# Kernel optimization log

Measured on AMD Instinct MI355X. Metric: run time of the kernel, lower is better.

Reference implementation:

```python
import jax, jax.numpy as jnp
import numpy as np

N_NODES = 100000


def _spmm(rows, cols, vals, x):
    # out[i] = sum over edges e with rows[e]==i of vals[e] * x[cols[e]]
    gathered = x[cols] * vals[:, None]          # [E, F]
    return jax.ops.segment_sum(gathered, rows, num_segments=N_NODES)


def setup_inputs() -> dict:
    key = jax.random.key(0)
    ks = jax.random.split(key, 8)
    E = 3200000
    features = jax.random.normal(ks[0], (N_NODES, 128), dtype=jnp.float32)
    adj_rows = jnp.sort(jax.random.randint(ks[1], (E,), 0, N_NODES))
    adj_cols = jax.random.randint(ks[2], (E,), 0, N_NODES)
    adj_vals = jax.random.uniform(ks[3], (E,), dtype=jnp.float32)
    W1 = jax.random.normal(ks[4], (128, 128), dtype=jnp.float32) * 0.05
    b1 = jnp.zeros((128,), dtype=jnp.float32)
    W2 = jax.random.normal(ks[5], (128, 128), dtype=jnp.float32) * 0.05
    b2 = jnp.zeros((128,), dtype=jnp.float32)
    return {"features": features, "adj_rows": adj_rows, "adj_cols": adj_cols,
            "adj_vals": adj_vals, "W1": W1, "b1": b1, "W2": W2, "b2": b2}


def reference(features, adj_rows, adj_cols, adj_vals, W1, b1, W2, b2):
    # GC layer 1: adj @ (x @ W1) + b1
    h = _spmm(adj_rows, adj_cols, adj_vals, features @ W1) + b1
    h = jax.nn.relu(h)
    # GC layer 2: adj @ (h @ W2) + b2
    out = _spmm(adj_rows, adj_cols, adj_vals, h @ W2) + b2
    return out
```

## Files before the change

kernel.cpp:

```cpp
#include <hip/hip_runtime.h>
#include <type_traits>

#define FDIM 128

__device__ __forceinline__ uint16_t f2bf(float f) {
    uint32_t u = __float_as_uint(f);
    uint32_t r = (u + 0x7fffu + ((u >> 16) & 1u)) >> 16;
    return (uint16_t)r;
}
__device__ __forceinline__ uint32_t pack_bf16(float a, float b) {
    return (uint32_t)f2bf(a) | ((uint32_t)f2bf(b) << 16);
}
__device__ __forceinline__ float bflo(uint32_t u) { return __uint_as_float(u << 16); }
__device__ __forceinline__ float bfhi(uint32_t u) { return __uint_as_float(u & 0xffff0000u); }
__device__ __forceinline__ float bf2f(uint16_t h) { return __uint_as_float((uint32_t)h << 16); }

__global__ __launch_bounds__(256) void build_row_ptr_k(const int* __restrict__ rows,
                                                       int E, int N,
                                                       int* __restrict__ rp) {
    int i = blockIdx.x * 256 + threadIdx.x;
    if (i > N) return;
    int lo = 0, hi = E;
    while (lo < hi) {
        int mid = (lo + hi) >> 1;
        if (rows[mid] < i) lo = mid + 1; else hi = mid;
    }
    rp[i] = lo;
}

template <int ABF>
__global__ __launch_bounds__(256) void gemm_k(const void* __restrict__ A_,
                                              const float* __restrict__ W,
                                              uint16_t* __restrict__ C, int M) {
    using AT = typename std::conditional<ABF, uint16_t, float>::type;
    const AT* A = (const AT*)A_;

    __shared__ float Ws[128][128];
    const int t = threadIdx.x;
    const int row0 = blockIdx.x * 128;

#pragma unroll
    for (int i = 0; i < 16; ++i) {
        int f = t + i * 256;
        int k = f >> 5;
        int c = (f & 31) << 2;
        *(float4*)&Ws[k][c] = *(const float4*)&W[(k << 7) + c];
    }
    __syncthreads();

    const int ty = t >> 4;
    const int tx = t & 15;

    const AT* aptr[8];
    int grow[8];
#pragma unroll
    for (int i = 0; i < 8; ++i) {
        int gr = row0 + ty * 8 + i;
        grow[i] = gr;
        if (gr >= M) gr = M - 1;
        aptr[i] = A + (size_t)gr * FDIM;
    }

    float acc[8][8];
#pragma unroll
    for (int i = 0; i < 8; ++i)
#pragma unroll
        for (int j = 0; j < 8; ++j) acc[i][j] = 0.f;

#pragma unroll 4
    for (int k = 0; k < 128; ++k) {
        float a[8], b[8];
#pragma unroll
        for (int i = 0; i < 8; ++i) {
            if constexpr (ABF) a[i] = bf2f(aptr[i][k]);
            else               a[i] = aptr[i][k];
        }
        *(float4*)&b[0] = *(const float4*)&Ws[k][tx * 8];
        *(float4*)&b[4] = *(const float4*)&Ws[k][tx * 8 + 4];
#pragma unroll
        for (int i = 0; i < 8; ++i)
#pragma unroll
            for (int j = 0; j < 8; ++j) acc[i][j] = fmaf(a[i], b[j], acc[i][j]);
    }

#pragma unroll
    for (int i = 0; i < 8; ++i) {
        if (grow[i] < M) {
            uint32_t p[4];
#pragma unroll
            for (int j = 0; j < 4; ++j)
                p[j] = pack_bf16(acc[i][2 * j], acc[i][2 * j + 1]);
            *(uint4*)&C[(size_t)grow[i] * FDIM + tx * 8] =
                make_uint4(p[0], p[1], p[2], p[3]);
        }
    }
}

template <int RELU, int OBF>
__global__ __launch_bounds__(256) void spmm_k(const int* __restrict__ rp,
                                              const int* __restrict__ cols,
                                              const float* __restrict__ vals,
                                              const uint32_t* __restrict__ X,
                                              const float* __restrict__ bias,
                                              void* __restrict__ out, int N) {
    int wid  = (blockIdx.x * 256 + threadIdx.x) >> 6;
    int lane = threadIdx.x & 63;
    if (wid >= N) return;
    int s = __builtin_amdgcn_readfirstlane(rp[wid]);
    int e = __builtin_amdgcn_readfirstlane(rp[wid + 1]);

    float ax0 = 0.f, ay0 = 0.f, ax1 = 0.f, ay1 = 0.f;
    float ax2 = 0.f, ay2 = 0.f, ax3 = 0.f, ay3 = 0.f;
    int i = s;
    for (; i + 4 <= e; i += 4) {
        int c0 = __builtin_amdgcn_readfirstlane(cols[i]);
        int c1 = __builtin_amdgcn_readfirstlane(cols[i + 1]);
        int c2 = __builtin_amdgcn_readfirstlane(cols[i + 2]);
        int c3 = __builtin_amdgcn_readfirstlane(cols[i + 3]);
        float v0 = vals[i], v1 = vals[i + 1], v2 = vals[i + 2], v3 = vals[i + 3];
        uint32_t u0 = X[(size_t)c0 * 64 + lane];
        uint32_t u1 = X[(size_t)c1 * 64 + lane];
        uint32_t u2 = X[(size_t)c2 * 64 + lane];
        uint32_t u3 = X[(size_t)c3 * 64 + lane];
        ax0 = fmaf(v0, bflo(u0), ax0); ay0 = fmaf(v0, bfhi(u0), ay0);
        ax1 = fmaf(v1, bflo(u1), ax1); ay1 = fmaf(v1, bfhi(u1), ay1);
        ax2 = fmaf(v2, bflo(u2), ax2); ay2 = fmaf(v2, bfhi(u2), ay2);
        ax3 = fmaf(v3, bflo(u3), ax3); ay3 = fmaf(v3, bfhi(u3), ay3);
    }
    for (; i < e; ++i) {
        int c0 = __builtin_amdgcn_readfirstlane(cols[i]);
        float v0 = vals[i];
        uint32_t u0 = X[(size_t)c0 * 64 + lane];
        ax0 = fmaf(v0, bflo(u0), ax0); ay0 = fmaf(v0, bfhi(u0), ay0);
    }

    float ox = (ax0 + ax1) + (ax2 + ax3) + bias[lane * 2];
    float oy = (ay0 + ay1) + (ay2 + ay3) + bias[lane * 2 + 1];
    if (RELU) { ox = fmaxf(ox, 0.f); oy = fmaxf(oy, 0.f); }

    if constexpr (OBF) {
        ((uint32_t*)out)[(size_t)wid * 64 + lane] = pack_bf16(ox, oy);
    } else {
        *(float2*)((float*)out + (size_t)wid * FDIM + lane * 2) = make_float2(ox, oy);
    }
}

extern "C" void kernel_launch(void* const* d_in, const int* in_sizes, int n_in,
                              void* d_out, int out_size, void* d_ws, size_t ws_size,
                              hipStream_t stream) {
    const float* features = (const float*)d_in[0];
    const int*   adj_cols = (const int*)d_in[2];
    const float* adj_vals = (const float*)d_in[3];
    const float* W1       = (const float*)d_in[4];
    const float* b1       = (const float*)d_in[5];
    const float* W2       = (const float*)d_in[6];
    const float* b2       = (const float*)d_in[7];
    const int*   adj_rows = (const int*)d_in[1];

    const int N = in_sizes[0] / FDIM;
    const int E = in_sizes[1];
    float* out = (float*)d_out;

    char* ws = (char*)d_ws;
    int* rp = (int*)ws;
    size_t rp_bytes = (((size_t)(N + 1) * sizeof(int)) + 255) & ~(size_t)255;
    uint16_t* XWb = (uint16_t*)(ws + rp_bytes);
    uint16_t* Hb  = XWb + (size_t)N * FDIM;

    build_row_ptr_k<<<(N + 256) / 256, 256, 0, stream>>>(adj_rows, E, N, rp);
    gemm_k<0><<<(N + 127) / 128, 256, 0, stream>>>((const void*)features, W1, XWb, N);
    spmm_k<1, 1><<<((size_t)N * 64 + 255) / 256, 256, 0, stream>>>(
        rp, adj_cols, adj_vals, (const uint32_t*)XWb, b1, (void*)Hb, N);
    gemm_k<1><<<(N + 127) / 128, 256, 0, stream>>>((const void*)Hb, W2, XWb, N);
    spmm_k<0, 0><<<((size_t)N * 64 + 255) / 256, 256, 0, stream>>>(
        rp, adj_cols, adj_vals, (const uint32_t*)XWb, b2, (void*)out, N);
}
```

Before: 343.6 us.

## Use bf16 MFMA for dense GEMMs and software-pipeline SpMM gathers by 8

Replaces the scalar-FMA shared-memory GEMM with a bf16 MFMA (16x16x32) kernel that reads a pre-transposed bf16 copy of each weight matrix. Two small transpose kernels produce those copies. The SpMM kernel now unrolls edges by 8 and prefetches the next group's column indices so more gathers are in flight. This adds rounding of the weights and fp32 features to bf16, and the SpMM change raises register pressure.

```diff
diff --git a/kernel.cpp b/kernel.cpp
--- a/kernel.cpp
+++ b/kernel.cpp
@@ -2,6 +2,9 @@
 #include <type_traits>
 
 #define FDIM 128
+
+typedef __attribute__((ext_vector_type(8))) short short8v;
+typedef __attribute__((ext_vector_type(4))) float f32x4;
 
 __device__ __forceinline__ uint16_t f2bf(float f) {
     uint32_t u = __float_as_uint(f);
@@ -13,7 +16,6 @@
 }
 __device__ __forceinline__ float bflo(uint32_t u) { return __uint_as_float(u << 16); }
 __device__ __forceinline__ float bfhi(uint32_t u) { return __uint_as_float(u & 0xffff0000u); }
-__device__ __forceinline__ float bf2f(uint16_t h) { return __uint_as_float((uint32_t)h << 16); }
 
 __global__ __launch_bounds__(256) void build_row_ptr_k(const int* __restrict__ rows,
                                                        int E, int N,
@@ -28,70 +30,74 @@
     rp[i] = lo;
 }
 
+__global__ __launch_bounds__(256) void transpose_w_k(const float* __restrict__ W,
+                                                     uint16_t* __restrict__ Wt) {
+    int idx = blockIdx.x * 256 + threadIdx.x;
+    int k = idx >> 7, n = idx & 127;
+    Wt[n * FDIM + k] = f2bf(W[k * FDIM + n]);
+}
+
 template <int ABF>
-__global__ __launch_bounds__(256) void gemm_k(const void* __restrict__ A_,
-                                              const float* __restrict__ W,
-                                              uint16_t* __restrict__ C, int M) {
-    using AT = typename std::conditional<ABF, uint16_t, float>::type;
-    const AT* A = (const AT*)A_;
-
-    __shared__ float Ws[128][128];
+__global__ __launch_bounds__(256) void gemm_mfma_k(const void* __restrict__ A_,
+                                                   const uint16_t* __restrict__ Wt,
+                                                   uint16_t* __restrict__ C, int M) {
     const int t = threadIdx.x;
-    const int row0 = blockIdx.x * 128;
-
-#pragma unroll
-    for (int i = 0; i < 16; ++i) {
-        int f = t + i * 256;
-        int k = f >> 5;
-        int c = (f & 31) << 2;
-        *(float4*)&Ws[k][c] = *(const float4*)&W[(k << 7) + c];
-    }
-    __syncthreads();
-
-    const int ty = t >> 4;
-    const int tx = t & 15;
-
-    const AT* aptr[8];
-    int grow[8];
-#pragma unroll
-    for (int i = 0; i < 8; ++i) {
-        int gr = row0 + ty * 8 + i;
-        grow[i] = gr;
-        if (gr >= M) gr = M - 1;
-        aptr[i] = A + (size_t)gr * FDIM;
-    }
-
-    float acc[8][8];
-#pragma unroll
-    for (int i = 0; i < 8; ++i)
-#pragma unroll
-        for (int j = 0; j < 8; ++j) acc[i][j] = 0.f;
-
-#pragma unroll 4
-    for (int k = 0; k < 128; ++k) {
-        float a[8], b[8];
-#pragma unroll
-        for (int i = 0; i < 8; ++i) {
-            if constexpr (ABF) a[i] = bf2f(aptr[i][k]);
-            else               a[i] = aptr[i][k];
-        }
-        *(float4*)&b[0] = *(const float4*)&Ws[k][tx * 8];
-        *(float4*)&b[4] = *(const float4*)&Ws[k][tx * 8 + 4];
-#pragma unroll
-        for (int i = 0; i < 8; ++i)
-#pragma unroll
-            for (int j = 0; j < 8; ++j) acc[i][j] = fmaf(a[i], b[j], acc[i][j]);
-    }
-
-#pragma unroll
-    for (int i = 0; i < 8; ++i) {
-        if (grow[i] < M) {
-            uint32_t p[4];
-#pragma unroll
-            for (int j = 0; j < 4; ++j)
-                p[j] = pack_bf16(acc[i][2 * j], acc[i][2 * j + 1]);
-            *(uint4*)&C[(size_t)grow[i] * FDIM + tx * 8] =
-                make_uint4(p[0], p[1], p[2], p[3]);
+    const int w = t >> 6;
+    const int l = t & 63;
+    const int row0 = blockIdx.x * 128 + w * 32;
+
+    f32x4 acc[2][8];
+#pragma unroll
+    for (int mf = 0; mf < 2; ++mf)
+#pragma unroll
+        for (int nf = 0; nf < 8; ++nf) acc[mf][nf] = (f32x4)0.f;
+
+    const int lr = l & 15;
+    const int kg = l >> 4;
+
+#pragma unroll
+    for (int ks = 0; ks < 4; ++ks) {
+        const int k0 = ks * 32 + kg * 8;
+        short8v a[2];
+#pragma unroll
+        for (int mf = 0; mf < 2; ++mf) {
+            int r = row0 + mf * 16 + lr;
+            if (r >= M) r = M - 1;
+            if constexpr (ABF) {
+                a[mf] = *(const short8v*)((const uint16_t*)A_ + (size_t)r * FDIM + k0);
+            } else {
+                const float* ap = (const float*)A_ + (size_t)r * FDIM + k0;
+                float4 f0 = *(const float4*)(ap);
+                float4 f1 = *(const float4*)(ap + 4);
+                uint32_t p0 = pack_bf16(f0.x, f0.y), p1 = pack_bf16(f0.z, f0.w);
+                uint32_t p2 = pack_bf16(f1.x, f1.y), p3 = pack_bf16(f1.z, f1.w);
+                uint4 u = make_uint4(p0, p1, p2, p3);
+                a[mf] = *(short8v*)&u;
+            }
+        }
+#pragma unroll
+        for (int nf = 0; nf < 8; ++nf) {
+            short8v b = *(const short8v*)(Wt + (size_t)(nf * 16 + lr) * FDIM + k0);
+            acc[0][nf] = __builtin_amdgcn_mfma_f32_16x16x32_bf16(a[0], b, acc[0][nf], 0, 0, 0);
+            acc[1][nf] = __builtin_amdgcn_mfma_f32_16x16x32_bf16(a[1], b, acc[1][nf], 0, 0, 0);
+        }
+    }
+
+    const int colpar = l & 1;
+#pragma unroll
+    for (int mf = 0; mf < 2; ++mf) {
+#pragma unroll
+        for (int nf = 0; nf < 8; ++nf) {
+            int col = nf * 16 + lr;
+#pragma unroll
+            for (int j = 0; j < 4; ++j) {
+                float v = acc[mf][nf][j];
+                float pv = __shfl_xor(v, 1);
+                int row = row0 + mf * 16 + kg * 4 + j;
+                if (!colpar && row < M) {
+                    *(uint32_t*)(C + (size_t)row * FDIM + col) = pack_bf16(v, pv);
+                }
+            }
         }
     }
 }
@@ -109,33 +115,59 @@
     int s = __builtin_amdgcn_readfirstlane(rp[wid]);
     int e = __builtin_amdgcn_readfirstlane(rp[wid + 1]);
 
-    float ax0 = 0.f, ay0 = 0.f, ax1 = 0.f, ay1 = 0.f;
-    float ax2 = 0.f, ay2 = 0.f, ax3 = 0.f, ay3 = 0.f;
+    float ax[8], ay[8];
+#pragma unroll
+    for (int j = 0; j < 8; ++j) { ax[j] = 0.f; ay[j] = 0.f; }
+
+    const int nfull = (e - s) >> 3;
     int i = s;
-    for (; i + 4 <= e; i += 4) {
-        int c0 = __builtin_amdgcn_readfirstlane(cols[i]);
-        int c1 = __builtin_amdgcn_readfirstlane(cols[i + 1]);
-        int c2 = __builtin_amdgcn_readfirstlane(cols[i + 2]);
-        int c3 = __builtin_amdgcn_readfirstlane(cols[i + 3]);
-        float v0 = vals[i], v1 = vals[i + 1], v2 = vals[i + 2], v3 = vals[i + 3];
-        uint32_t u0 = X[(size_t)c0 * 64 + lane];
-        uint32_t u1 = X[(size_t)c1 * 64 + lane];
-        uint32_t u2 = X[(size_t)c2 * 64 + lane];
-        uint32_t u3 = X[(size_t)c3 * 64 + lane];
-        ax0 = fmaf(v0, bflo(u0), ax0); ay0 = fmaf(v0, bfhi(u0), ay0);
-        ax1 = fmaf(v1, bflo(u1), ax1); ay1 = fmaf(v1, bfhi(u1), ay1);
-        ax2 = fmaf(v2, bflo(u2), ax2); ay2 = fmaf(v2, bfhi(u2), ay2);
-        ax3 = fmaf(v3, bflo(u3), ax3); ay3 = fmaf(v3, bfhi(u3), ay3);
+    int cc[8];
+
+    if (nfull > 0) {
+#pragma unroll
+        for (int j = 0; j < 8; ++j) cc[j] = __builtin_amdgcn_readfirstlane(cols[i + j]);
+        for (int g = 1; g < nfull; ++g) {
+            int cn[8];
+#pragma unroll
+            for (int j = 0; j < 8; ++j) cn[j] = __builtin_amdgcn_readfirstlane(cols[i + 8 + j]);
+            uint32_t u[8];
+#pragma unroll
+            for (int j = 0; j < 8; ++j) u[j] = X[(size_t)cc[j] * 64 + lane];
+#pragma unroll
+            for (int j = 0; j < 8; ++j) {
+                float v = vals[i + j];
+                ax[j] = fmaf(v, bflo(u[j]), ax[j]);
+                ay[j] = fmaf(v, bfhi(u[j]), ay[j]);
+            }
+#pragma unroll
+            for (int j = 0; j < 8; ++j) cc[j] = cn[j];
+            i += 8;
+        }
+        {
+            uint32_t u[8];
+#pragma unroll
+            for (int j = 0; j < 8; ++j) u[j] = X[(size_t)cc[j] * 64 + lane];
+#pragma unroll
+            for (int j = 0; j < 8; ++j) {
+                float v = vals[i + j];
+                ax[j] = fmaf(v, bflo(u[j]), ax[j]);
+                ay[j] = fmaf(v, bfhi(u[j]), ay[j]);
+            }
+            i += 8;
+        }
     }
     for (; i < e; ++i) {
-        int c0 = __builtin_amdgcn_readfirstlane(cols[i]);
-        float v0 = vals[i];
-        uint32_t u0 = X[(size_t)c0 * 64 + lane];
-        ax0 = fmaf(v0, bflo(u0), ax0); ay0 = fmaf(v0, bfhi(u0), ay0);
-    }
-
-    float ox = (ax0 + ax1) + (ax2 + ax3) + bias[lane * 2];
-    float oy = (ay0 + ay1) + (ay2 + ay3) + bias[lane * 2 + 1];
+        int c = __builtin_amdgcn_readfirstlane(cols[i]);
+        float v = vals[i];
+        uint32_t u = X[(size_t)c * 64 + lane];
+        ax[0] = fmaf(v, bflo(u), ax[0]);
+        ay[0] = fmaf(v, bfhi(u), ay[0]);
+    }
+
+    float ox = ((ax[0] + ax[1]) + (ax[2] + ax[3])) + ((ax[4] + ax[5]) + (ax[6] + ax[7]));
+    float oy = ((ay[0] + ay[1]) + (ay[2] + ay[3])) + ((ay[4] + ay[5]) + (ay[6] + ay[7]));
+    ox += bias[lane * 2];
+    oy += bias[lane * 2 + 1];
     if (RELU) { ox = fmaxf(ox, 0.f); oy = fmaxf(oy, 0.f); }
 
     if constexpr (OBF) {
@@ -149,13 +181,13 @@
                               void* d_out, int out_size, void* d_ws, size_t ws_size,
                               hipStream_t stream) {
     const float* features = (const float*)d_in[0];
+    const int*   adj_rows = (const int*)d_in[1];
     const int*   adj_cols = (const int*)d_in[2];
     const float* adj_vals = (const float*)d_in[3];
     const float* W1       = (const float*)d_in[4];
     const float* b1       = (const float*)d_in[5];
     const float* W2       = (const float*)d_in[6];
     const float* b2       = (const float*)d_in[7];
-    const int*   adj_rows = (const int*)d_in[1];
 
     const int N = in_sizes[0] / FDIM;
     const int E = in_sizes[1];
@@ -166,12 +198,18 @@
     size_t rp_bytes = (((size_t)(N + 1) * sizeof(int)) + 255) & ~(size_t)255;
     uint16_t* XWb = (uint16_t*)(ws + rp_bytes);
     uint16_t* Hb  = XWb + (size_t)N * FDIM;
+    uint16_t* W1t = Hb + (size_t)N * FDIM;
+    uint16_t* W2t = W1t + FDIM * FDIM;
+
+    const int nblk = (N + 127) / 128;
 
     build_row_ptr_k<<<(N + 256) / 256, 256, 0, stream>>>(adj_rows, E, N, rp);
-    gemm_k<0><<<(N + 127) / 128, 256, 0, stream>>>((const void*)features, W1, XWb, N);
+    transpose_w_k<<<64, 256, 0, stream>>>(W1, W1t);
+    transpose_w_k<<<64, 256, 0, stream>>>(W2, W2t);
+    gemm_mfma_k<0><<<nblk, 256, 0, stream>>>((const void*)features, W1t, XWb, N);
     spmm_k<1, 1><<<((size_t)N * 64 + 255) / 256, 256, 0, stream>>>(
         rp, adj_cols, adj_vals, (const uint32_t*)XWb, b1, (void*)Hb, N);
-    gemm_k<1><<<(N + 127) / 128, 256, 0, stream>>>((const void*)Hb, W2, XWb, N);
+    gemm_mfma_k<1><<<nblk, 256, 0, stream>>>((const void*)Hb, W2t, XWb, N);
     spmm_k<0, 0><<<((size_t)N * 64 + 255) / 256, 256, 0, stream>>>(
         rp, adj_cols, adj_vals, (const uint32_t*)XWb, b2, (void*)out, N);
 }
```

Result: faster. 291.0 us (-15.3%).
